# Optimization experiments

Measured on AMD Instinct MI355X. Metric: run time of the kernel, lower is better.

Reference implementation:

```python
import jax, jax.numpy as jnp
import numpy as np

E = 1024
H = 16          # num_heads
D = E // H      # head_dim
HID = 1024      # hidden_dim
B, S = 16, 512
EPS = 1e-5


def _ln(x, g, b):
    mu = jnp.mean(x, axis=-1, keepdims=True)
    var = jnp.mean(jnp.square(x - mu), axis=-1, keepdims=True)
    return (x - mu) * jax.lax.rsqrt(var + EPS) * g + b


def setup_inputs() -> dict:
    key = jax.random.key(0)
    ks = jax.random.split(key, 8)
    s = 1.0 / np.sqrt(E)
    return {
        'state_features': jax.random.normal(ks[0], (6, B, S, E), jnp.float32),
        'Wq': jax.random.normal(ks[1], (E, E), jnp.float32) * s,
        'bq': jnp.zeros((E,), jnp.float32),
        'Wk': jax.random.normal(ks[2], (E, E), jnp.float32) * s,
        'bk': jnp.zeros((E,), jnp.float32),
        'Wv': jax.random.normal(ks[3], (E, E), jnp.float32) * s,
        'bv': jnp.zeros((E,), jnp.float32),
        'Wo': jax.random.normal(ks[4], (E, E), jnp.float32) * s,
        'bo': jnp.zeros((E,), jnp.float32),
        'ln1_g': jnp.ones((E,), jnp.float32),
        'ln1_b': jnp.zeros((E,), jnp.float32),
        'fusion_w': jnp.ones((6,), jnp.float32) / 6.0,
        'Wf': jax.random.normal(ks[5], (HID, E), jnp.float32) * s,
        'bf': jnp.zeros((HID,), jnp.float32),
        'ln2_g': jnp.ones((HID,), jnp.float32),
        'ln2_b': jnp.zeros((HID,), jnp.float32),
    }


def reference(state_features, Wq, bq, Wk, bk, Wv, bv, Wo, bo,
              ln1_g, ln1_b, fusion_w, Wf, bf, ln2_g, ln2_b):
    # state_features: (6, B, S, E) -> stacked (N, 6, E), N = B*S
    st = jnp.transpose(state_features, (1, 2, 0, 3)).reshape(B * S, 6, E)
    N = st.shape[0]

    q = (st @ Wq.T + bq).reshape(N, 6, H, D)
    k = (st @ Wk.T + bk).reshape(N, 6, H, D)
    v = (st @ Wv.T + bv).reshape(N, 6, H, D)

    # tiny 6x6 attention per token per head (dropout = identity in eval)
    scores = jnp.einsum('nqhd,nkhd->nhqk', q, k) / np.sqrt(D).astype(np.float32)
    attn = jax.nn.softmax(scores, axis=-1)
    ctx = jnp.einsum('nhqk,nkhd->nqhd', attn, v).reshape(N, 6, E)

    out = ctx @ Wo.T + bo
    enhanced = _ln(out + st, ln1_g, ln1_b)  # (N, 6, E)

    # weighted_sum fusion
    w = jax.nn.softmax(fusion_w)
    fused = jnp.einsum('nse,s->ne', enhanced, w)

    hidden = fused @ Wf.T + bf
    hidden = jnp.where(hidden >= 0, hidden, 0.01 * hidden)  # LeakyReLU(0.01)
    hidden = _ln(hidden, ln2_g, ln2_b)
    return hidden.reshape(B, S, HID)
```

## Files before the change

### kernel.cpp

```cpp
#include <hip/hip_runtime.h>
#include <hip/hip_bf16.h>

#define NTOK 8192
#define E 1024
#define NS 6
#define MBIG (NTOK * NS)
#define NSE ((long)NTOK * E)

typedef short short8 __attribute__((ext_vector_type(8)));
typedef float f32x4 __attribute__((ext_vector_type(4)));
typedef unsigned short ushort4v __attribute__((ext_vector_type(4)));

#define TM 128
#define TN 128
#define BK 64

static __device__ __forceinline__ float bf2f(unsigned short u) {
    union { unsigned int i; float f; } c; c.i = ((unsigned int)u) << 16; return c.f;
}

struct WPtrs { const float* s[5]; __hip_bfloat16* d[5]; };
__global__ __launch_bounds__(256) void cvt5_w(WPtrs p)
{
    const int seg = blockIdx.x >> 10;
    const int i = ((blockIdx.x & 1023) * 256 + threadIdx.x) * 4;
    const float4 v = *(const float4*)(p.s[seg] + i);
    union { __hip_bfloat16 h[4]; unsigned long long u; } pk;
    pk.h[0] = (__hip_bfloat16)v.x;
    pk.h[1] = (__hip_bfloat16)v.y;
    pk.h[2] = (__hip_bfloat16)v.z;
    pk.h[3] = (__hip_bfloat16)v.w;
    *(unsigned long long*)(p.d[seg] + i) = pk.u;
}

__global__ __launch_bounds__(256) void cvt_bulk(
    const float* __restrict__ src, __hip_bfloat16* __restrict__ dst)
{
    const long i = ((long)blockIdx.x * 256 + threadIdx.x) * 4;
    const float4 v = *(const float4*)(src + i);
    union { __hip_bfloat16 h[4]; unsigned long long u; } pk;
    pk.h[0] = (__hip_bfloat16)v.x;
    pk.h[1] = (__hip_bfloat16)v.y;
    pk.h[2] = (__hip_bfloat16)v.z;
    pk.h[3] = (__hip_bfloat16)v.w;
    *(unsigned long long*)(dst + i) = pk.u;
}

#define NITER  8

struct GOut { __hip_bfloat16* C[3]; const float* bias[3]; };

static __device__ __forceinline__ void stage_half(
    const __hip_bfloat16* gsrc,
    __hip_bfloat16* ldst, int tid)
{
#pragma unroll
    for (int piece = 0; piece < 2; ++piece) {
        const int r  = piece * 64 + (tid >> 3);
        const int s  = tid & 7;
        const int ss = s ^ (r & 7);
        const __hip_bfloat16* g = gsrc + (long)r * 1024 + ss * 8;
        __hip_bfloat16* l = ldst + r * 64 + s * 8;
        __builtin_amdgcn_global_load_lds((const __attribute__((address_space(1))) void*)g,
                                         (__attribute__((address_space(3))) void*)l, 16, 0, 0);
    }
}

static __device__ __forceinline__ short8 ld_frag(
    const __hip_bfloat16* half_base, int lr, int slot)
{
    return *(const short8*)(half_base + lr * 64 + ((slot ^ (lr & 7)) << 3));
}

#define STAGE(kt, part)                                                         \
  {                                                                             \
    const int _b  = (kt) & 1;                                                   \
    const int _ab = (part) >> 1;                                                \
    const int _hf = (part) & 1;                                                 \
    const __hip_bfloat16* _g = (_ab == 0)                                       \
        ? A  + (m0 + _hf * 128) * 1024 + (kt) * 64                              \
        : Wb + ((long)n0 + _hf * 128) * 1024 + (kt) * 64;                       \
    stage_half(_g, &lds[((_b * 2 + _ab) * 2 + _hf) * 8192], tid);               \
  }

#define PHASE(kt, q, STMT_STAGE, STMT_WAIT)                                     \
  {                                                                             \
    const int _buf = (kt) & 1;                                                  \
    const __hip_bfloat16* _Ab = &lds[((_buf * 2 + 0) * 2 + wm) * 8192];         \
    const __hip_bfloat16* _Bb = &lds[((_buf * 2 + 1) * 2 + (wn >> 1)) * 8192];  \
    if ((q) == 0) {                                                             \
      _Pragma("unroll") for (int nf = 0; nf < 4; ++nf)                          \
        _Pragma("unroll") for (int k2 = 0; k2 < 2; ++k2)                        \
          bfr[nf][k2] = ld_frag(_Bb, (wn & 1) * 64 + nf * 16 + mrow,            \
                                k2 * 4 + quad);                                 \
    }                                                                           \
    _Pragma("unroll") for (int mf = 0; mf < 2; ++mf)                            \
      _Pragma("unroll") for (int k2 = 0; k2 < 2; ++k2)                          \
        afr[mf][k2] = ld_frag(_Ab, (q) * 32 + mf * 16 + mrow, k2 * 4 + quad);   \
    STMT_STAGE;                                                                 \
    STMT_WAIT;                                                                  \
    __builtin_amdgcn_s_barrier();                                               \
    asm volatile("s_waitcnt lgkmcnt(0)" ::: "memory");                          \
    __builtin_amdgcn_sched_barrier(0);                                          \
    __builtin_amdgcn_s_setprio(1);                                              \
    _Pragma("unroll") for (int mf = 0; mf < 2; ++mf)                            \
      _Pragma("unroll") for (int nf = 0; nf < 4; ++nf)                          \
        _Pragma("unroll") for (int k2 = 0; k2 < 2; ++k2)                        \
          acc[(q) * 2 + mf][nf] = __builtin_amdgcn_mfma_f32_16x16x32_bf16(      \
              bfr[nf][k2], afr[mf][k2], acc[(q) * 2 + mf][nf], 0, 0, 0);        \
    __builtin_amdgcn_s_setprio(0);                                              \
    __builtin_amdgcn_s_barrier();                                               \
  }

__global__ __launch_bounds__(512) void gemm256(
    const __hip_bfloat16* __restrict__ A,
    const __hip_bfloat16* __restrict__ Wb,
    GOut out)
{
    __shared__ __hip_bfloat16 lds[2 * 2 * 2 * 8192] __attribute__((aligned(16)));

    const int tid  = threadIdx.x;
    const int lane = tid & 63;
    const int wid  = tid >> 6;
    const int quad = lane >> 4;
    const int mrow = lane & 15;
    const int wm = wid >> 2;
    const int wn = wid & 3;

    const int gx  = gridDim.x;
    const int nwg = gx * gridDim.y;
    const int cpx = nwg >> 3;
    const int lin = blockIdx.y * gx + blockIdx.x;
    const int tile = (lin & 7) * cpx + (lin >> 3);
    const int  n0 = (tile % gx) * 256;
    const long m0 = (long)(tile / gx) * 256;

    f32x4 acc[8][4] = {};
    short8 bfr[4][2];
    short8 afr[2][2];

    STAGE(0, 0); STAGE(0, 1); STAGE(0, 2); STAGE(0, 3);
    STAGE(1, 2); STAGE(1, 3);
    asm volatile("s_waitcnt vmcnt(4)" ::: "memory");
    __builtin_amdgcn_s_barrier();

#pragma unroll 1
    for (int it = 0; it < NITER; ++it) {
        const int kt0 = 2 * it;
        const int kt1 = 2 * it + 1;
        const bool more = (it < NITER - 1);

        PHASE(kt0, 0, STAGE(kt1, 0), ((void)0));
        PHASE(kt0, 1, STAGE(kt1, 1), ((void)0));
        PHASE(kt0, 2, if (more) STAGE(kt0 + 2, 2), ((void)0));
        PHASE(kt0, 3, if (more) STAGE(kt0 + 2, 3),
              if (more) { asm volatile("s_waitcnt vmcnt(4)" ::: "memory"); }
              else      { asm volatile("s_waitcnt vmcnt(0)" ::: "memory"); });
        PHASE(kt1, 0, if (more) STAGE(kt0 + 2, 0), ((void)0));
        PHASE(kt1, 1, if (more) STAGE(kt0 + 2, 1), ((void)0));
        PHASE(kt1, 2, if (more) STAGE(kt0 + 3, 2), ((void)0));
        PHASE(kt1, 3, if (more) STAGE(kt0 + 3, 3),
              if (more) { asm volatile("s_waitcnt vmcnt(4)" ::: "memory"); });
    }

    const int seg = n0 >> 10;
    const int nb  = n0 & 1023;
    __hip_bfloat16* Cp = out.C[seg];
    const float* bp = out.bias[seg];
#pragma unroll
    for (int mf = 0; mf < 8; ++mf) {
        const long row = m0 + wm * 128 + mf * 16 + mrow;
#pragma unroll
        for (int nf = 0; nf < 4; ++nf) {
            const int colb = nb + wn * 64 + nf * 16 + quad * 4;
            const f32x4 bv4 = *(const f32x4*)(bp + colb);
            union { __hip_bfloat16 h[4]; unsigned long long u; } pk;
#pragma unroll
            for (int r = 0; r < 4; ++r)
                pk.h[r] = (__hip_bfloat16)(acc[mf][nf][r] + bv4[r]);
            *(unsigned long long*)(Cp + row * 1024 + colb) = pk.u;
        }
    }
}

__global__ __launch_bounds__(256) void gemm_bt(
    const __hip_bfloat16* __restrict__ A,
    const __hip_bfloat16* __restrict__ Wb,
    const float* __restrict__ bias,
    __hip_bfloat16* __restrict__ C)
{
    __shared__ __hip_bfloat16 lA[TM * BK] __attribute__((aligned(16)));
    __shared__ __hip_bfloat16 lB[TN * BK] __attribute__((aligned(16)));

    const int tid  = threadIdx.x;
    const int wave = tid >> 6;
    const int lane = tid & 63;
    const int quad = lane >> 4;
    const int mrow = lane & 15;
    const int wr = wave >> 1;
    const int wc = wave & 1;

    const int Gy   = gridDim.y;
    const int lin  = blockIdx.y * 8 + blockIdx.x;
    const int tile = (lin & 7) * Gy + (lin >> 3);
    const int  n0 = (tile & 7) * TN;
    const long m0 = (long)(tile >> 3) * TM;

    const int srow = lane >> 3;
    const int scol = (lane & 7) * 8;

    f32x4 acc[4][4] = {};

    for (int k0 = 0; k0 < 1024; k0 += BK) {
        __syncthreads();
#pragma unroll
        for (int it = 0; it < 4; ++it) {
            const int chunk = it * 4 + wave;
            const int row   = chunk * 8 + srow;
            const __hip_bfloat16* ga = A + (m0 + row) * 1024 + k0 + scol;
            const __hip_bfloat16* gb = Wb + (long)(n0 + row) * 1024 + k0 + scol;
            __hip_bfloat16* la = lA + row * BK + scol;
            __hip_bfloat16* lb = lB + row * BK + scol;
            __builtin_amdgcn_global_load_lds((const __attribute__((address_space(1))) void*)ga,
                                             (__attribute__((address_space(3))) void*)la, 16, 0, 0);
            __builtin_amdgcn_global_load_lds((const __attribute__((address_space(1))) void*)gb,
                                             (__attribute__((address_space(3))) void*)lb, 16, 0, 0);
        }
        __syncthreads();

#pragma unroll
        for (int kk = 0; kk < BK; kk += 32) {
            short8 af[4], bfrg[4];
#pragma unroll
            for (int i = 0; i < 4; ++i)
                af[i] = *(const short8*)(lA + (wr * 64 + i * 16 + mrow) * BK + kk + quad * 8);
#pragma unroll
            for (int j = 0; j < 4; ++j)
                bfrg[j] = *(const short8*)(lB + (wc * 64 + j * 16 + mrow) * BK + kk + quad * 8);
#pragma unroll
            for (int i = 0; i < 4; ++i)
#pragma unroll
                for (int j = 0; j < 4; ++j)
                    acc[i][j] = __builtin_amdgcn_mfma_f32_16x16x32_bf16(af[i], bfrg[j], acc[i][j], 0, 0, 0);
        }
    }

#pragma unroll
    for (int i = 0; i < 4; ++i) {
#pragma unroll
        for (int j = 0; j < 4; ++j) {
            const int col = n0 + wc * 64 + j * 16 + mrow;
            const float bv = bias[col];
#pragma unroll
            for (int r = 0; r < 4; ++r) {
                const long row = m0 + wr * 64 + i * 16 + quad * 4 + r;
                C[row * 1024 + col] = (__hip_bfloat16)(acc[i][j][r] + bv);
            }
        }
    }
}

__global__ __launch_bounds__(256) void gemm_a32_bt(
    const float* __restrict__ A,
    const __hip_bfloat16* __restrict__ Wb,
    const float* __restrict__ bias,
    __hip_bfloat16* __restrict__ C)
{
    __shared__ __hip_bfloat16 lA[TM * BK] __attribute__((aligned(16)));
    __shared__ __hip_bfloat16 lB[TN * BK] __attribute__((aligned(16)));

    const int tid  = threadIdx.x;
    const int wave = tid >> 6;
    const int lane = tid & 63;
    const int quad = lane >> 4;
    const int mrow = lane & 15;
    const int wr = wave >> 1;
    const int wc = wave & 1;

    const int Gy   = gridDim.y;
    const int lin  = blockIdx.y * 8 + blockIdx.x;
    const int tile = (lin & 7) * Gy + (lin >> 3);
    const int  n0 = (tile & 7) * TN;
    const long m0 = (long)(tile >> 3) * TM;

    const int srow = lane >> 3;
    const int scol = (lane & 7) * 8;

    f32x4 acc[4][4] = {};

    for (int k0 = 0; k0 < 1024; k0 += BK) {
        __syncthreads();
#pragma unroll
        for (int it = 0; it < 4; ++it) {
            const int chunk = it * 4 + wave;
            const int row   = chunk * 8 + srow;
            const __hip_bfloat16* gb = Wb + (long)(n0 + row) * 1024 + k0 + scol;
            __hip_bfloat16* lb = lB + row * BK + scol;
            __builtin_amdgcn_global_load_lds((const __attribute__((address_space(1))) void*)gb,
                                             (__attribute__((address_space(3))) void*)lb, 16, 0, 0);
        }
#pragma unroll
        for (int u = 0; u < 8; ++u) {
            const int c   = u * 256 + tid;
            const int row = c >> 4;
            const int c4  = c & 15;
            const float4 av = *(const float4*)(A + (m0 + row) * 1024 + k0 + c4 * 4);
            union { __hip_bfloat16 h[4]; unsigned long long uu; } pk;
            pk.h[0] = (__hip_bfloat16)av.x;
            pk.h[1] = (__hip_bfloat16)av.y;
            pk.h[2] = (__hip_bfloat16)av.z;
            pk.h[3] = (__hip_bfloat16)av.w;
            *(unsigned long long*)(lA + row * BK + c4 * 4) = pk.uu;
        }
        __syncthreads();

#pragma unroll
        for (int kk = 0; kk < BK; kk += 32) {
            short8 af[4], bfrg[4];
#pragma unroll
            for (int i = 0; i < 4; ++i)
                af[i] = *(const short8*)(lA + (wr * 64 + i * 16 + mrow) * BK + kk + quad * 8);
#pragma unroll
            for (int j = 0; j < 4; ++j)
                bfrg[j] = *(const short8*)(lB + (wc * 64 + j * 16 + mrow) * BK + kk + quad * 8);
#pragma unroll
            for (int i = 0; i < 4; ++i)
#pragma unroll
                for (int j = 0; j < 4; ++j)
                    acc[i][j] = __builtin_amdgcn_mfma_f32_16x16x32_bf16(af[i], bfrg[j], acc[i][j], 0, 0, 0);
        }
    }

#pragma unroll
    for (int i = 0; i < 4; ++i) {
#pragma unroll
        for (int j = 0; j < 4; ++j) {
            const int col = n0 + wc * 64 + j * 16 + mrow;
            const float bv = bias[col];
#pragma unroll
            for (int r = 0; r < 4; ++r) {
                const long row = m0 + wr * 64 + i * 16 + quad * 4 + r;
                C[row * 1024 + col] = (__hip_bfloat16)(acc[i][j][r] + bv);
            }
        }
    }
}

__global__ __launch_bounds__(256) void attn6(
    const __hip_bfloat16* qb,
    const __hip_bfloat16* __restrict__ kb,
    const __hip_bfloat16* __restrict__ vb,
    __hip_bfloat16* ctx)
{
    const int w    = blockIdx.x * 4 + (threadIdx.x >> 6);
    const int lane = threadIdx.x & 63;
    const int n  = w >> 2;
    const int hg = w & 3;
    const int h  = hg * 4 + (lane >> 4);
    const int sub = lane & 15;
    const long base = (long)n * 1024 + h * 64 + sub * 4;

    float qf[NS][4], kf[NS][4], vf[NS][4];
#pragma unroll
    for (int s = 0; s < NS; ++s) {
        const ushort4v qs = *(const ushort4v*)(qb + s * NSE + base);
        const ushort4v ks = *(const ushort4v*)(kb + s * NSE + base);
        const ushort4v vs = *(const ushort4v*)(vb + s * NSE + base);
#pragma unroll
        for (int c = 0; c < 4; ++c) {
            qf[s][c] = bf2f(qs[c]);
            kf[s][c] = bf2f(ks[c]);
            vf[s][c] = bf2f(vs[c]);
        }
    }

    float p[NS][NS];
#pragma unroll
    for (int i = 0; i < NS; ++i)
#pragma unroll
        for (int j = 0; j < NS; ++j) {
            float t = qf[i][0] * kf[j][0];
            t = fmaf(qf[i][1], kf[j][1], t);
            t = fmaf(qf[i][2], kf[j][2], t);
            t = fmaf(qf[i][3], kf[j][3], t);
            t += __shfl_xor(t, 1, 64);
            t += __shfl_xor(t, 2, 64);
            t += __shfl_xor(t, 4, 64);
            t += __shfl_xor(t, 8, 64);
            p[i][j] = t * 0.125f;
        }

#pragma unroll
    for (int i = 0; i < NS; ++i) {
        float m = p[i][0];
#pragma unroll
        for (int j = 1; j < NS; ++j) m = fmaxf(m, p[i][j]);
        float sum = 0.f;
#pragma unroll
        for (int j = 0; j < NS; ++j) { p[i][j] = __expf(p[i][j] - m); sum += p[i][j]; }
        const float inv = 1.0f / sum;
        float a[4] = {0.f, 0.f, 0.f, 0.f};
#pragma unroll
        for (int j = 0; j < NS; ++j)
#pragma unroll
            for (int c = 0; c < 4; ++c) a[c] = fmaf(p[i][j], vf[j][c], a[c]);
        union { __hip_bfloat16 h4[4]; unsigned long long u; } pk;
#pragma unroll
        for (int c = 0; c < 4; ++c) pk.h4[c] = (__hip_bfloat16)(a[c] * inv);
        *(unsigned long long*)(ctx + i * NSE + base) = pk.u;
    }
}

__global__ __launch_bounds__(256) void ln1_fuse(
    const __hip_bfloat16* __restrict__ wo_out,
    const float* __restrict__ sf,
    const float* __restrict__ g,
    const float* __restrict__ b,
    const float* __restrict__ fw,
    __hip_bfloat16* __restrict__ fused)
{
    const int n = blockIdx.x, tid = threadIdx.x;
    const int wave = tid >> 6, lane = tid & 63;
    const int e0 = tid * 4;

    float w[NS];
    float mx = -1e30f;
#pragma unroll
    for (int s = 0; s < NS; ++s) { w[s] = fw[s]; mx = fmaxf(mx, w[s]); }
    float sw = 0.f;
#pragma unroll
    for (int s = 0; s < NS; ++s) { w[s] = __expf(w[s] - mx); sw += w[s]; }
    const float isw = 1.0f / sw;

    const f32x4 gv4 = *(const f32x4*)(g + e0);
    const f32x4 bv4 = *(const f32x4*)(b + e0);

    __shared__ float red[2][4];
    float accf[4] = {0.f, 0.f, 0.f, 0.f};

    for (int s = 0; s < NS; ++s) {
        const long base = s * NSE + (long)n * 1024 + e0;
        const ushort4v wv = *(const ushort4v*)(wo_out + base);
        const f32x4   sv = *(const f32x4*)(sf + base);
        float x[4];
        float sum = 0.f, sq = 0.f;
#pragma unroll
        for (int c = 0; c < 4; ++c) {
            x[c] = bf2f(wv[c]) + sv[c];
            sum += x[c];
            sq  += x[c] * x[c];
        }
#pragma unroll
        for (int off = 32; off; off >>= 1) {
            sum += __shfl_xor(sum, off, 64);
            sq  += __shfl_xor(sq,  off, 64);
        }
        if (lane == 0) { red[0][wave] = sum; red[1][wave] = sq; }
        __syncthreads();
        sum = red[0][0] + red[0][1] + red[0][2] + red[0][3];
        sq  = red[1][0] + red[1][1] + red[1][2] + red[1][3];
        __syncthreads();
        const float mu   = sum * (1.0f / 1024.0f);
        const float var  = sq * (1.0f / 1024.0f) - mu * mu;
        const float rstd = rsqrtf(var + 1e-5f);
        const float ws_  = w[s] * isw;
#pragma unroll
        for (int c = 0; c < 4; ++c)
            accf[c] += ws_ * ((x[c] - mu) * rstd * gv4[c] + bv4[c]);
    }
    union { __hip_bfloat16 h4[4]; unsigned long long u; } pk;
#pragma unroll
    for (int c = 0; c < 4; ++c) pk.h4[c] = (__hip_bfloat16)accf[c];
    *(unsigned long long*)(fused + (long)n * 1024 + e0) = pk.u;
}

__global__ __launch_bounds__(256) void ln2_out(
    const __hip_bfloat16* __restrict__ hidden,
    const float* __restrict__ g,
    const float* __restrict__ b,
    float* __restrict__ out)
{
    const int n = blockIdx.x, tid = threadIdx.x;
    const int wave = tid >> 6, lane = tid & 63;
    const int e0 = tid * 4;
    __shared__ float red[2][4];

    const ushort4v hv = *(const ushort4v*)(hidden + (long)n * 1024 + e0);
    float x[4];
    float sum = 0.f, sq = 0.f;
#pragma unroll
    for (int c = 0; c < 4; ++c) {
        float t = bf2f(hv[c]);
        t = t >= 0.f ? t : 0.01f * t;
        x[c] = t;
        sum += t;
        sq  += t * t;
    }
#pragma unroll
    for (int off = 32; off; off >>= 1) {
        sum += __shfl_xor(sum, off, 64);
        sq  += __shfl_xor(sq,  off, 64);
    }
    if (lane == 0) { red[0][wave] = sum; red[1][wave] = sq; }
    __syncthreads();
    sum = red[0][0] + red[0][1] + red[0][2] + red[0][3];
    sq  = red[1][0] + red[1][1] + red[1][2] + red[1][3];
    const float mu   = sum * (1.0f / 1024.0f);
    const float var  = sq * (1.0f / 1024.0f) - mu * mu;
    const float rstd = rsqrtf(var + 1e-5f);

    const f32x4 gv4 = *(const f32x4*)(g + e0);
    const f32x4 bv4 = *(const f32x4*)(b + e0);
    f32x4 o;
#pragma unroll
    for (int c = 0; c < 4; ++c)
        o[c] = (x[c] - mu) * rstd * gv4[c] + bv4[c];
    *(f32x4*)(out + (long)n * 1024 + e0) = o;
}

extern "C" void kernel_launch(void* const* d_in, const int* in_sizes, int n_in,
                              void* d_out, int out_size, void* d_ws, size_t ws_size,
                              hipStream_t stream)
{
    const float* SF  = (const float*)d_in[0];
    const float* Wq  = (const float*)d_in[1];
    const float* bq  = (const float*)d_in[2];
    const float* Wk  = (const float*)d_in[3];
    const float* bk  = (const float*)d_in[4];
    const float* Wv  = (const float*)d_in[5];
    const float* bv  = (const float*)d_in[6];
    const float* Wo  = (const float*)d_in[7];
    const float* bo  = (const float*)d_in[8];
    const float* g1  = (const float*)d_in[9];
    const float* b1  = (const float*)d_in[10];
    const float* fw  = (const float*)d_in[11];
    const float* Wf  = (const float*)d_in[12];
    const float* bf_ = (const float*)d_in[13];
    const float* g2  = (const float*)d_in[14];
    const float* b2  = (const float*)d_in[15];
    float* out = (float*)d_out;

    const size_t REG = (size_t)MBIG * 1024 * sizeof(__hip_bfloat16);
    const size_t WTS = (size_t)5 * 1024 * 1024 * sizeof(__hip_bfloat16);
    const bool big_ws = ws_size >= 4 * REG + WTS;

    __hip_bfloat16* r0  = (__hip_bfloat16*)d_ws;
    __hip_bfloat16* r1  = r0 + (long)MBIG * 1024;
    __hip_bfloat16* r2  = r1 + (long)MBIG * 1024;
    __hip_bfloat16* r3  = r2 + (long)MBIG * 1024;
    __hip_bfloat16* wb  = big_ws ? (r3 + (long)MBIG * 1024) : r3;
    __hip_bfloat16* Wqb = wb;
    __hip_bfloat16* Wkb = Wqb + 1024 * 1024;
    __hip_bfloat16* Wvb = Wkb + 1024 * 1024;
    __hip_bfloat16* Wob = Wvb + 1024 * 1024;
    __hip_bfloat16* Wfb = Wob + 1024 * 1024;

    const dim3 blk(256);

    WPtrs wp;
    wp.s[0] = Wq; wp.s[1] = Wk; wp.s[2] = Wv; wp.s[3] = Wo; wp.s[4] = Wf;
    wp.d[0] = Wqb; wp.d[1] = Wkb; wp.d[2] = Wvb; wp.d[3] = Wob; wp.d[4] = Wfb;
    cvt5_w<<<5 * 1024, blk, 0, stream>>>(wp);

    cvt_bulk<<<MBIG, blk, 0, stream>>>(SF, r2);

    if (big_ws) {
        const dim3 blk2(512);
        const dim3 gQKV(12, MBIG / 256);
        const dim3 gB2(4, MBIG / 256);

        GOut oqkv;
        oqkv.C[0] = r0; oqkv.C[1] = r1; oqkv.C[2] = r3;
        oqkv.bias[0] = bq; oqkv.bias[1] = bk; oqkv.bias[2] = bv;
        gemm256<<<gQKV, blk2, 0, stream>>>(r2, Wqb, oqkv);

        attn6<<<NTOK, blk, 0, stream>>>(r0, r1, r3, r0);

        GOut owo;
        owo.C[0] = r1; owo.C[1] = r1; owo.C[2] = r1;
        owo.bias[0] = bo; owo.bias[1] = bo; owo.bias[2] = bo;
        gemm256<<<gB2, blk2, 0, stream>>>(r0, Wob, owo);

        ln1_fuse<<<NTOK, blk, 0, stream>>>(r1, SF, g1, b1, fw, r2);

        gemm_bt<<<dim3(8, NTOK / TM), blk, 0, stream>>>(r2, Wfb, bf_, r0);

        ln2_out<<<NTOK, blk, 0, stream>>>(r0, g2, b2, out);
    } else {
        const dim3 gBig(8, MBIG / TM);
        const dim3 gSm(8, NTOK / TM);

        gemm_bt<<<gBig, blk, 0, stream>>>(r2, Wqb, bq, r0);
        gemm_bt<<<gBig, blk, 0, stream>>>(r2, Wkb, bk, r1);
        gemm_a32_bt<<<gBig, blk, 0, stream>>>(SF, Wvb, bv, r2);
        attn6<<<NTOK, blk, 0, stream>>>(r0, r1, r2, r0);
        gemm_bt<<<gBig, blk, 0, stream>>>(r0, Wob, bo, r1);
        ln1_fuse<<<NTOK, blk, 0, stream>>>(r1, SF, g1, b1, fw, r2);
        gemm_bt<<<gSm, blk, 0, stream>>>(r2, Wfb, bf_, r0);
        ln2_out<<<NTOK, blk, 0, stream>>>(r0, g2, b2, out);
    }
}
```

Measured before the change: 928.3 us.

## Prefetch LDS fragments one phase ahead and use 256-tile GEMM for final projection

```diff
diff --git a/kernel.cpp b/kernel.cpp
--- a/kernel.cpp
+++ b/kernel.cpp
@@ -83,20 +83,8 @@
     stage_half(_g, &lds[((_b * 2 + _ab) * 2 + _hf) * 8192], tid);               \
   }
 
-#define PHASE(kt, q, STMT_STAGE, STMT_WAIT)                                     \
+#define PH(kt, q, HASNEXT, nkt, STMT_STAGE, STMT_WAIT)                          \
   {                                                                             \
-    const int _buf = (kt) & 1;                                                  \
-    const __hip_bfloat16* _Ab = &lds[((_buf * 2 + 0) * 2 + wm) * 8192];         \
-    const __hip_bfloat16* _Bb = &lds[((_buf * 2 + 1) * 2 + (wn >> 1)) * 8192];  \
-    if ((q) == 0) {                                                             \
-      _Pragma("unroll") for (int nf = 0; nf < 4; ++nf)                          \
-        _Pragma("unroll") for (int k2 = 0; k2 < 2; ++k2)                        \
-          bfr[nf][k2] = ld_frag(_Bb, (wn & 1) * 64 + nf * 16 + mrow,            \
-                                k2 * 4 + quad);                                 \
-    }                                                                           \
-    _Pragma("unroll") for (int mf = 0; mf < 2; ++mf)                            \
-      _Pragma("unroll") for (int k2 = 0; k2 < 2; ++k2)                          \
-        afr[mf][k2] = ld_frag(_Ab, (q) * 32 + mf * 16 + mrow, k2 * 4 + quad);   \
     STMT_STAGE;                                                                 \
     STMT_WAIT;                                                                  \
     __builtin_amdgcn_s_barrier();                                               \
@@ -107,8 +95,26 @@
       _Pragma("unroll") for (int nf = 0; nf < 4; ++nf)                          \
         _Pragma("unroll") for (int k2 = 0; k2 < 2; ++k2)                        \
           acc[(q) * 2 + mf][nf] = __builtin_amdgcn_mfma_f32_16x16x32_bf16(      \
-              bfr[nf][k2], afr[mf][k2], acc[(q) * 2 + mf][nf], 0, 0, 0);        \
+              bfr[nf][k2], afr[(q) & 1][mf][k2], acc[(q) * 2 + mf][nf], 0,0,0); \
     __builtin_amdgcn_s_setprio(0);                                              \
+    if ((q) < 3) {                                                              \
+      const __hip_bfloat16* _Ab = &lds[((((kt) & 1) * 2 + 0) * 2 + wm) * 8192]; \
+      _Pragma("unroll") for (int mf = 0; mf < 2; ++mf)                          \
+        _Pragma("unroll") for (int k2 = 0; k2 < 2; ++k2)                        \
+          afr[((q) + 1) & 1][mf][k2] =                                          \
+              ld_frag(_Ab, ((q) + 1) * 32 + mf * 16 + mrow, k2 * 4 + quad);     \
+    } else if (HASNEXT) {                                                       \
+      const __hip_bfloat16* _An = &lds[((((nkt) & 1) * 2 + 0) * 2 + wm) * 8192];\
+      const __hip_bfloat16* _Bn =                                               \
+          &lds[((((nkt) & 1) * 2 + 1) * 2 + (wn >> 1)) * 8192];                 \
+      _Pragma("unroll") for (int nf = 0; nf < 4; ++nf)                          \
+        _Pragma("unroll") for (int k2 = 0; k2 < 2; ++k2)                        \
+          bfr[nf][k2] = ld_frag(_Bn, (wn & 1) * 64 + nf * 16 + mrow,            \
+                                k2 * 4 + quad);                                 \
+      _Pragma("unroll") for (int mf = 0; mf < 2; ++mf)                          \
+        _Pragma("unroll") for (int k2 = 0; k2 < 2; ++k2)                        \
+          afr[0][mf][k2] = ld_frag(_An, mf * 16 + mrow, k2 * 4 + quad);         \
+    }                                                                           \
     __builtin_amdgcn_s_barrier();                                               \
   }
 
@@ -137,12 +143,27 @@
 
     f32x4 acc[8][4] = {};
     short8 bfr[4][2];
-    short8 afr[2][2];
+    short8 afr[2][2][2];
 
     STAGE(0, 0); STAGE(0, 1); STAGE(0, 2); STAGE(0, 3);
     STAGE(1, 2); STAGE(1, 3);
     asm volatile("s_waitcnt vmcnt(4)" ::: "memory");
     __builtin_amdgcn_s_barrier();
+
+    {
+        const __hip_bfloat16* _Ab = &lds[(0 * 2 + wm) * 8192];
+        const __hip_bfloat16* _Bb = &lds[((0 * 2 + 1) * 2 + (wn >> 1)) * 8192];
+#pragma unroll
+        for (int nf = 0; nf < 4; ++nf)
+#pragma unroll
+            for (int k2 = 0; k2 < 2; ++k2)
+                bfr[nf][k2] = ld_frag(_Bb, (wn & 1) * 64 + nf * 16 + mrow, k2 * 4 + quad);
+#pragma unroll
+        for (int mf = 0; mf < 2; ++mf)
+#pragma unroll
+            for (int k2 = 0; k2 < 2; ++k2)
+                afr[0][mf][k2] = ld_frag(_Ab, mf * 16 + mrow, k2 * 4 + quad);
+    }
 
 #pragma unroll 1
     for (int it = 0; it < NITER; ++it) {
@@ -150,17 +171,17 @@
         const int kt1 = 2 * it + 1;
         const bool more = (it < NITER - 1);
 
-        PHASE(kt0, 0, STAGE(kt1, 0), ((void)0));
-        PHASE(kt0, 1, STAGE(kt1, 1), ((void)0));
-        PHASE(kt0, 2, if (more) STAGE(kt0 + 2, 2), ((void)0));
-        PHASE(kt0, 3, if (more) STAGE(kt0 + 2, 3),
-              if (more) { asm volatile("s_waitcnt vmcnt(4)" ::: "memory"); }
-              else      { asm volatile("s_waitcnt vmcnt(0)" ::: "memory"); });
-        PHASE(kt1, 0, if (more) STAGE(kt0 + 2, 0), ((void)0));
-        PHASE(kt1, 1, if (more) STAGE(kt0 + 2, 1), ((void)0));
-        PHASE(kt1, 2, if (more) STAGE(kt0 + 3, 2), ((void)0));
-        PHASE(kt1, 3, if (more) STAGE(kt0 + 3, 3),
-              if (more) { asm volatile("s_waitcnt vmcnt(4)" ::: "memory"); });
+        PH(kt0, 0, true, kt0, STAGE(kt1, 0), ((void)0));
+        PH(kt0, 1, true, kt0, STAGE(kt1, 1), ((void)0));
+        PH(kt0, 2, true, kt0, if (more) STAGE(kt0 + 2, 2), ((void)0));
+        PH(kt0, 3, true, kt1, if (more) STAGE(kt0 + 2, 3),
+           if (more) { asm volatile("s_waitcnt vmcnt(4)" ::: "memory"); }
+           else      { asm volatile("s_waitcnt vmcnt(0)" ::: "memory"); });
+        PH(kt1, 0, true, kt1, if (more) STAGE(kt0 + 2, 0), ((void)0));
+        PH(kt1, 1, true, kt1, if (more) STAGE(kt0 + 2, 1), ((void)0));
+        PH(kt1, 2, true, kt1, if (more) STAGE(kt0 + 3, 2), ((void)0));
+        PH(kt1, 3, more, kt0 + 2, if (more) STAGE(kt0 + 3, 3),
+           if (more) { asm volatile("s_waitcnt vmcnt(4)" ::: "memory"); });
     }
 
     const int seg = n0 >> 10;
@@ -568,6 +589,7 @@
         const dim3 blk2(512);
         const dim3 gQKV(12, MBIG / 256);
         const dim3 gB2(4, MBIG / 256);
+        const dim3 gSm2(4, NTOK / 256);
 
         GOut oqkv;
         oqkv.C[0] = r0; oqkv.C[1] = r1; oqkv.C[2] = r3;
@@ -583,7 +605,10 @@
 
         ln1_fuse<<<NTOK, blk, 0, stream>>>(r1, SF, g1, b1, fw, r2);
 
-        gemm_bt<<<dim3(8, NTOK / TM), blk, 0, stream>>>(r2, Wfb, bf_, r0);
+        GOut owf;
+        owf.C[0] = r0; owf.C[1] = r0; owf.C[2] = r0;
+        owf.bias[0] = bf_; owf.bias[1] = bf_; owf.bias[2] = bf_;
+        gemm256<<<gSm2, blk2, 0, stream>>>(r2, Wfb, owf);
 
         ln2_out<<<NTOK, blk, 0, stream>>>(r0, g2, b2, out);
     } else {
```

Result: no change. 928.5 us (+0.0%).
